# Performance work log

Hardware: AMD Instinct MI355X
Metric: run time of the kernel (lower is better)

## Reference

```python
import jax, jax.numpy as jnp
import numpy as np

B, C, H, W = 2, 192, 64, 64
HEADS, KS = 6, 7
HD = C // HEADS


def setup_inputs() -> dict:
    key = jax.random.key(0)
    ks = jax.random.split(key, 6)
    s = 0.02
    return {
        "x": jax.random.normal(ks[0], (B, C, H, W), jnp.float32),
        "W_qkv1": jax.random.normal(ks[1], (3 * C, C, 1, 1), jnp.float32) * s,
        "b_qkv1": jnp.zeros((3 * C,), jnp.float32),
        "W_qkv2": jax.random.normal(ks[2], (3 * C, 1, 3, 3), jnp.float32) * s,  # depthwise
        "b_qkv2": jnp.zeros((3 * C,), jnp.float32),
        "temperature": jnp.ones((HEADS, 1, 1, 1), jnp.float32),
        "rpb": jax.random.normal(ks[3], (HEADS, 2 * KS - 1, 2 * KS - 1), jnp.float32) * s,
        "W_proj": jax.random.normal(ks[4], (C, C, 1, 1), jnp.float32) * s,
        "b_proj": jnp.zeros((C,), jnp.float32),
    }


def _conv(x, w, b, pad, groups=1):
    y = jax.lax.conv_general_dilated(
        x, w, (1, 1), pad,
        dimension_numbers=("NCHW", "OIHW", "NCHW"),
        feature_group_count=groups)
    return y + b[None, :, None, None]


def _l2norm(t, eps=1e-12):
    n = jnp.sqrt(jnp.sum(t * t, axis=-1, keepdims=True))
    return t / jnp.maximum(n, eps)


def _nbr_idx(L, K):
    # NATTEN shifted-window neighborhood (dilation=1): window start clamped to image.
    start = jnp.clip(jnp.arange(L) - K // 2, 0, L - K)
    idx = start[:, None] + jnp.arange(K)[None, :]        # [L,K] absolute neighbor index
    rel = idx - jnp.arange(L)[:, None] + (K - 1)         # [L,K] rpb table index
    return idx, rel


def _forward(x, W_qkv1, b_qkv1, W_qkv2, b_qkv2, temperature, rpb, W_proj, b_proj):
    Bq, Cq, Hh, Ww = x.shape
    heads = rpb.shape[0]
    K = (rpb.shape[1] + 1) // 2
    hd = Cq // heads
    qkv = _conv(_conv(x, W_qkv1, b_qkv1, "VALID"), W_qkv2, b_qkv2, "SAME", groups=3 * Cq)
    qkv = qkv.reshape(Bq, 3, heads, hd, Hh, Ww).transpose(1, 0, 2, 4, 5, 3)  # [3,B,h,H,W,d]
    q, k, v = qkv[0], qkv[1], qkv[2]
    q = _l2norm(q)
    k = _l2norm(k)
    idx_i, rel_i = _nbr_idx(Hh, K)
    idx_j, rel_j = _nbr_idx(Ww, K)
    ii = idx_i[:, None, :, None]  # [H,1,K,1]
    jj = idx_j[None, :, None, :]  # [1,W,1,K] -> broadcast [H,W,K,K]
    k_nb = k[:, :, ii, jj, :]     # [B,h,H,W,K,K,d]
    attn = jnp.einsum("bhijd,bhijkld->bhijkl", q, k_nb)
    bias = rpb[:, rel_i[:, None, :, None], rel_j[None, :, None, :]]  # [h,H,W,K,K]
    attn = (attn + bias[None]) * temperature.reshape(1, heads, 1, 1, 1, 1)
    attn = jax.nn.softmax(attn.reshape(Bq, heads, Hh, Ww, K * K), axis=-1)
    v_nb = v[:, :, ii, jj, :].reshape(Bq, heads, Hh, Ww, K * K, hd)
    out = jnp.einsum("bhijk,bhijkd->bhijd", attn, v_nb)
    out = out.transpose(0, 1, 4, 2, 3).reshape(Bq, Cq, Hh, Ww)
    return _conv(out, W_proj, b_proj, "VALID")


def reference(x, W_qkv1, b_qkv1, W_qkv2, b_qkv2, temperature, rpb, W_proj, b_proj):
    return _forward(x, W_qkv1, b_qkv1, W_qkv2, b_qkv2, temperature, rpb, W_proj, b_proj)
```

## Files before the change

### kernel.cpp

```cpp
#include <hip/hip_runtime.h>
#include <math.h>

#define HW 4096

typedef __attribute__((ext_vector_type(8))) short short8;
typedef __attribute__((ext_vector_type(8))) _Float16 half8;
typedef __attribute__((ext_vector_type(4))) float floatx4;

__device__ inline float bflo(unsigned u) { return __uint_as_float(u << 16); }
__device__ inline float bfhi(unsigned u) { return __uint_as_float(u & 0xffff0000u); }
__device__ inline unsigned short f2bf(float x) {
    unsigned u = __float_as_uint(x);
    return (unsigned short)((u + 0x7fffu + ((u >> 16) & 1u)) >> 16);
}
__device__ inline unsigned f2bf2(float lo, float hi) {
    unsigned a = __float_as_uint(lo), b = __float_as_uint(hi);
    a = (a + 0x7fffu + ((a >> 16) & 1u)) >> 16;
    b = (b + 0x7fffu + ((b >> 16) & 1u)) & 0xffff0000u;
    return a | b;
}
__device__ inline unsigned short f2h(float x) {
    _Float16 h = (_Float16)x;
    return __builtin_bit_cast(unsigned short, h);
}


__global__ __launch_bounds__(256) void k_gq(const float* __restrict__ x,
    const float* __restrict__ W1, const float* __restrict__ b1,
    unsigned short* __restrict__ qkv)
{
    __shared__ __align__(16) unsigned short As[64 * 200];
    __shared__ __align__(16) unsigned short Bs[64 * 200];
    const int t = threadIdx.x;
    const int m0 = blockIdx.x * 64;
    const int n0 = blockIdx.y * 64;
    const int w = t >> 6, lane = t & 63;
    const int b = m0 >> 12, px0 = m0 & 4095;
    {
        const float* xb = x + ((size_t)(b * 192) << 12) + px0 + lane;
        const int cb = w * 48;
        #pragma unroll
        for (int r4 = 0; r4 < 12; ++r4) {
            float v0 = xb[(size_t)(cb + r4 * 4 + 0) << 12];
            float v1 = xb[(size_t)(cb + r4 * 4 + 1) << 12];
            float v2 = xb[(size_t)(cb + r4 * 4 + 2) << 12];
            float v3 = xb[(size_t)(cb + r4 * 4 + 3) << 12];
            *(uint2*)&As[lane * 200 + cb + r4 * 4] =
                make_uint2(f2bf2(v0, v1), f2bf2(v2, v3));
        }
    }
    #pragma unroll
    for (int pass = 0; pass < 12; ++pass) {
        int idx = pass * 256 + t;
        int row = idx / 48, ch = idx - row * 48;
        float4 wv = *(const float4*)&W1[(size_t)(n0 + row) * 192 + ch * 4];
        *(uint2*)&Bs[row * 200 + ch * 4] =
            make_uint2(f2bf2(wv.x, wv.y), f2bf2(wv.z, wv.w));
    }
    __syncthreads();
    const int lm = lane & 15, lq = lane >> 4;
    floatx4 acc[4] = {};
    #pragma unroll
    for (int ks = 0; ks < 6; ++ks) {
        short8 bf = *(const short8*)&Bs[(w * 16 + lm) * 200 + ks * 32 + lq * 8];
        #pragma unroll
        for (int mt = 0; mt < 4; ++mt) {
            short8 af = *(const short8*)&As[(mt * 16 + lm) * 200 + ks * 32 + lq * 8];
            acc[mt] = __builtin_amdgcn_mfma_f32_16x16x32_bf16(af, bf, acc[mt], 0, 0, 0);
        }
    }
    __syncthreads();
    const float bias = b1[n0 + w * 16 + lm];
    #pragma unroll
    for (int mt = 0; mt < 4; ++mt)
        #pragma unroll
        for (int r = 0; r < 4; ++r)
            As[(mt * 16 + lq * 4 + r) * 72 + w * 16 + lm] = f2bf(acc[mt][r] + bias);
    __syncthreads();
    #pragma unroll
    for (int pass = 0; pass < 2; ++pass) {
        int idx = pass * 256 + t;
        int m = idx >> 3, n8 = idx & 7;
        uint4 val = *(const uint4*)&As[m * 72 + n8 * 8];
        int oc = n0 + n8 * 8;
        int g = oc >> 5, d = oc & 31;
        *(uint4*)&qkv[((((size_t)(b * 18 + g) << 12) + px0 + m) << 5) + d] = val;
    }
}

__global__ __launch_bounds__(256) void k_attn(const unsigned short* __restrict__ qkv,
    const float* __restrict__ W2, const float* __restrict__ b2,
    const float* __restrict__ temp, const float* __restrict__ rpb,
    unsigned short* __restrict__ attnO)
{
    __shared__ __align__(16) char lds[49088];
    unsigned short* Ks  = (unsigned short*)lds;
    unsigned short* Ps  = (unsigned short*)lds;
    unsigned short* Vts = (unsigned short*)(lds + 29696);
    float* rpbs = (float*)(lds + 44544);
    float* dwW  = (float*)(lds + 45248);
    float* dwB  = (float*)(lds + 48704);

    const int t = threadIdx.x;
    const int head = blockIdx.y, b = blockIdx.z;

    for (int idx = t; idx < 864; idx += 256) {
        int plane = idx / 288, rem = idx - plane * 288;
        dwW[idx] = W2[(plane * 192 + head * 32 + (rem & 31)) * 9 + (rem >> 5)];
    }
    if (t < 96) dwB[t] = b2[(t >> 5) * 192 + head * 32 + (t & 31)];
    if (t < 169) rpbs[t] = rpb[head * 169 + t];
    __syncthreads();

    const int ti = blockIdx.x >> 3, tj = blockIdx.x & 7;
    const int i0 = ti * 8, j0 = tj * 8;
    const int r0 = min(max(i0 - 3, 0), 50), c0 = min(max(j0 - 3, 0), 50);
    const unsigned short* qpl = qkv + ((size_t)(b * 18 + head) << 17);
    const unsigned short* kpl = qkv + ((size_t)(b * 18 + 6 + head) << 17);
    const unsigned short* vpl = qkv + ((size_t)(b * 18 + 12 + head) << 17);

    if (t < 196) {
        int r = (t * 2341) >> 15, cc = t - r * 14;
        const int pi = r0 + r, pj = c0 + cc;
        float acc[32];
        #pragma unroll
        for (int e = 0; e < 32; ++e) acc[e] = dwB[32 + e];
        #pragma unroll
        for (int di = -1; di <= 1; ++di) {
            int ii = pi + di;
            if (ii < 0 || ii > 63) continue;
            #pragma unroll
            for (int dj = -1; dj <= 1; ++dj) {
                int jj = pj + dj;
                if (jj < 0 || jj > 63) continue;
                const float* wt = &dwW[(9 + (di + 1) * 3 + dj + 1) * 32];
                const uint4* kg = (const uint4*)(kpl + (((ii << 6) + jj) << 5));
                #pragma unroll
                for (int q = 0; q < 4; ++q) {
                    uint4 u = kg[q];
                    unsigned uu[4] = {u.x, u.y, u.z, u.w};
                    #pragma unroll
                    for (int e = 0; e < 4; ++e) {
                        acc[q * 8 + e * 2]     = fmaf(bflo(uu[e]), wt[q * 8 + e * 2],     acc[q * 8 + e * 2]);
                        acc[q * 8 + e * 2 + 1] = fmaf(bfhi(uu[e]), wt[q * 8 + e * 2 + 1], acc[q * 8 + e * 2 + 1]);
                    }
                }
            }
        }
        float ss = 0.f;
        #pragma unroll
        for (int e = 0; e < 32; ++e) ss = fmaf(acc[e], acc[e], ss);
        float rinv = 1.0f / fmaxf(sqrtf(ss), 1e-12f);
        #pragma unroll
        for (int q = 0; q < 4; ++q) {
            uint4 p;
            p.x = f2bf2(acc[q * 8 + 0] * rinv, acc[q * 8 + 1] * rinv);
            p.y = f2bf2(acc[q * 8 + 2] * rinv, acc[q * 8 + 3] * rinv);
            p.z = f2bf2(acc[q * 8 + 4] * rinv, acc[q * 8 + 5] * rinv);
            p.w = f2bf2(acc[q * 8 + 6] * rinv, acc[q * 8 + 7] * rinv);
            *(uint4*)&Ks[t * 40 + q * 8] = p;
        }
        #pragma unroll
        for (int e = 0; e < 32; ++e) acc[e] = dwB[64 + e];
        #pragma unroll
        for (int di = -1; di <= 1; ++di) {
            int ii = pi + di;
            if (ii < 0 || ii > 63) continue;
            #pragma unroll
            for (int dj = -1; dj <= 1; ++dj) {
                int jj = pj + dj;
                if (jj < 0 || jj > 63) continue;
                const float* wt = &dwW[(18 + (di + 1) * 3 + dj + 1) * 32];
                const uint4* vg = (const uint4*)(vpl + (((ii << 6) + jj) << 5));
                #pragma unroll
                for (int q = 0; q < 4; ++q) {
                    uint4 u = vg[q];
                    unsigned uu[4] = {u.x, u.y, u.z, u.w};
                    #pragma unroll
                    for (int e = 0; e < 4; ++e) {
                        acc[q * 8 + e * 2]     = fmaf(bflo(uu[e]), wt[q * 8 + e * 2],     acc[q * 8 + e * 2]);
                        acc[q * 8 + e * 2 + 1] = fmaf(bfhi(uu[e]), wt[q * 8 + e * 2 + 1], acc[q * 8 + e * 2 + 1]);
                    }
                }
            }
        }
        #pragma unroll
        for (int e = 0; e < 32; ++e) Vts[e * 232 + t] = f2h(acc[e]);
    }
    for (int idx = t; idx < 448; idx += 256) {
        int row = (idx * 2341) >> 15;
        int c = idx - row * 14;
        ((unsigned*)(Vts + row * 232))[98 + c] = 0u;
    }

    const int w = t >> 6, lane = t & 63;
    const int lm = lane & 15, lq = lane >> 4;
    const int px = w * 16 + lm;
    const int i = i0 + (px >> 3), j = j0 + (px & 7);
    float qf[8];
    #pragma unroll
    for (int e = 0; e < 8; ++e) qf[e] = dwB[lq * 8 + e];
    #pragma unroll
    for (int di = -1; di <= 1; ++di) {
        int ii = i + di;
        if (ii < 0 || ii > 63) continue;
        #pragma unroll
        for (int dj = -1; dj <= 1; ++dj) {
            int jj = j + dj;
            if (jj < 0 || jj > 63) continue;
            const float* wt = &dwW[((di + 1) * 3 + dj + 1) * 32 + lq * 8];
            uint4 u = *(const uint4*)(qpl + ((((ii << 6) + jj) << 5) + lq * 8));
            unsigned uu[4] = {u.x, u.y, u.z, u.w};
            #pragma unroll
            for (int e = 0; e < 4; ++e) {
                qf[e * 2]     = fmaf(bflo(uu[e]), wt[e * 2],     qf[e * 2]);
                qf[e * 2 + 1] = fmaf(bfhi(uu[e]), wt[e * 2 + 1], qf[e * 2 + 1]);
            }
        }
    }
    float qs = 0.f;
    #pragma unroll
    for (int e = 0; e < 8; ++e) qs = fmaf(qf[e], qf[e], qs);
    qs += __shfl_xor(qs, 16);
    qs += __shfl_xor(qs, 32);
    float qinv = 1.0f / fmaxf(sqrtf(qs), 1e-12f);
    short8 bq;
    #pragma unroll
    for (int e = 0; e < 8; ++e) bq[e] = (short)f2bf(qf[e] * qinv);
    __syncthreads();

    floatx4 acc[13];
    #pragma unroll
    for (int mt = 0; mt < 13; ++mt) {
        short8 ak = *(const short8*)&Ks[(mt * 16 + lm) * 40 + lq * 8];
        floatx4 z = {0.f, 0.f, 0.f, 0.f};
        acc[mt] = __builtin_amdgcn_mfma_f32_16x16x32_bf16(ak, bq, z, 0, 0, 0);
    }
    __syncthreads();

    const int si = min(max(i - 3, 0), 57), sj = min(max(j - 3, 0), 57);
    const int vloi = si - r0, vloj = sj - c0;
    const int oi = r0 - i + 6, oj = c0 - j + 6;
    const float th = temp[head];
    float mx = -1e30f;
    #pragma unroll
    for (int mt = 0; mt < 13; ++mt) {
        int nb0 = mt * 16 + lq * 4;
        int rh0 = (nb0 * 2341) >> 15;
        int ch0 = nb0 - rh0 * 14;
        #pragma unroll
        for (int r = 0; r < 4; ++r) {
            int ch = ch0 + r, rh = rh0;
            if (ch >= 14) { ch -= 14; rh += 1; }
            int bidx = (rh + oi) * 13 + (ch + oj);
            float bias = rpbs[max(0, min(168, bidx))];
            bool valid = ((unsigned)(rh - vloi) <= 6u) && ((unsigned)(ch - vloj) <= 6u);
            float s = (acc[mt][r] + bias) * th;
            s = valid ? s : -1e30f;
            acc[mt][r] = s;
            mx = fmaxf(mx, s);
        }
    }
    mx = fmaxf(mx, __shfl_xor(mx, 16));
    mx = fmaxf(mx, __shfl_xor(mx, 32));
    float ssum = 0.f;
    #pragma unroll
    for (int mt = 0; mt < 13; ++mt)
        #pragma unroll
        for (int r = 0; r < 4; ++r) {
            float e = __expf(acc[mt][r] - mx);
            acc[mt][r] = e;
            ssum += e;
        }
    ssum += __shfl_xor(ssum, 16);
    ssum += __shfl_xor(ssum, 32);
    const float rs = 1.0f / ssum;

    if (lane < 32) {
        uint4 z4 = {0u, 0u, 0u, 0u};
        *(uint4*)&Ps[(w * 16 + (lane >> 1)) * 232 + 208 + (lane & 1) * 8] = z4;
    }
    #pragma unroll
    for (int mt = 0; mt < 13; ++mt) {
        unsigned lo = (unsigned)f2h(acc[mt][0] * rs) | ((unsigned)f2h(acc[mt][1] * rs) << 16);
        unsigned hi = (unsigned)f2h(acc[mt][2] * rs) | ((unsigned)f2h(acc[mt][3] * rs) << 16);
        *(uint2*)&Ps[px * 232 + mt * 16 + lq * 4] = make_uint2(lo, hi);
    }
    __syncthreads();

    floatx4 oacc[2] = {};
    #pragma unroll
    for (int ks = 0; ks < 7; ++ks) {
        half8 ap = *(const half8*)&Ps[(w * 16 + lm) * 232 + ks * 32 + lq * 8];
        #pragma unroll
        for (int n2 = 0; n2 < 2; ++n2) {
            half8 bv = *(const half8*)&Vts[(n2 * 16 + lm) * 232 + ks * 32 + lq * 8];
            oacc[n2] = __builtin_amdgcn_mfma_f32_16x16x32_f16(ap, bv, oacc[n2], 0, 0, 0);
        }
    }
    #pragma unroll
    for (int n2 = 0; n2 < 2; ++n2)
        #pragma unroll
        for (int r = 0; r < 4; ++r) {
            int p2 = w * 16 + lq * 4 + r;
            int i2 = i0 + (p2 >> 3), j2 = j0 + (p2 & 7);
            attnO[((size_t)((b << 12) + (i2 << 6) + j2)) * 192 + head * 32 + n2 * 16 + lm]
                = f2bf(oacc[n2][r]);
        }
}

__global__ __launch_bounds__(256) void k_gp(const unsigned short* __restrict__ Ain,
    const float* __restrict__ Wp, const float* __restrict__ bp,
    float* __restrict__ out)
{
    __shared__ __align__(16) unsigned short As[64 * 200];
    __shared__ __align__(16) unsigned short Bs[64 * 200];
    const int t = threadIdx.x;
    const int m0 = blockIdx.x * 64;
    const int n0 = blockIdx.y * 64;
    #pragma unroll
    for (int pass = 0; pass < 6; ++pass) {
        int idx = pass * 256 + t;
        int m = idx / 24, c16 = idx % 24;
        *(uint4*)&As[m * 200 + c16 * 8] = *(const uint4*)&Ain[(size_t)(m0 + m) * 192 + c16 * 8];
    }
    #pragma unroll
    for (int pass = 0; pass < 12; ++pass) {
        int idx = pass * 256 + t;
        int row = idx / 48, ch = idx - row * 48;
        float4 wv = *(const float4*)&Wp[(size_t)(n0 + row) * 192 + ch * 4];
        *(uint2*)&Bs[row * 200 + ch * 4] =
            make_uint2(f2bf2(wv.x, wv.y), f2bf2(wv.z, wv.w));
    }
    __syncthreads();
    const int w = t >> 6, lane = t & 63;
    const int lm = lane & 15, lq = lane >> 4;
    floatx4 acc[4] = {};
    #pragma unroll
    for (int ks = 0; ks < 6; ++ks) {
        short8 bf = *(const short8*)&Bs[(w * 16 + lm) * 200 + ks * 32 + lq * 8];
        #pragma unroll
        for (int mt = 0; mt < 4; ++mt) {
            short8 af = *(const short8*)&As[(mt * 16 + lm) * 200 + ks * 32 + lq * 8];
            acc[mt] = __builtin_amdgcn_mfma_f32_16x16x32_bf16(af, bf, acc[mt], 0, 0, 0);
        }
    }
    __syncthreads();
    float* fs = (float*)As;
    const float bias = bp[n0 + w * 16 + lm];
    #pragma unroll
    for (int mt = 0; mt < 4; ++mt)
        #pragma unroll
        for (int r = 0; r < 4; ++r)
            fs[(w * 16 + lm) * 68 + mt * 16 + lq * 4 + r] = acc[mt][r] + bias;
    __syncthreads();
    const int b = m0 >> 12, px0 = m0 & 4095;
    #pragma unroll
    for (int pass = 0; pass < 4; ++pass) {
        int idx = pass * 256 + t;
        int n = idx >> 4, m4 = idx & 15;
        float4 val = *(const float4*)&fs[n * 68 + m4 * 4];
        *(float4*)&out[((size_t)(b * 192 + n0 + n) << 12) + px0 + m4 * 4] = val;
    }
}

extern "C" void kernel_launch(void* const* d_in, const int* in_sizes, int n_in,
                              void* d_out, int out_size, void* d_ws, size_t ws_size,
                              hipStream_t stream) {
    const float* x    = (const float*)d_in[0];
    const float* W1   = (const float*)d_in[1];
    const float* b1   = (const float*)d_in[2];
    const float* W2   = (const float*)d_in[3];
    const float* b2   = (const float*)d_in[4];
    const float* temp = (const float*)d_in[5];
    const float* rpb  = (const float*)d_in[6];
    const float* Wp   = (const float*)d_in[7];
    const float* bp   = (const float*)d_in[8];
    float* out = (float*)d_out;

    char* ws = (char*)d_ws;
    unsigned short* qkv1b = (unsigned short*)(ws);
    unsigned short* attnO = (unsigned short*)(ws + 9437184);

    k_gq  <<<dim3(128, 9), 256, 0, stream>>>(x, W1, b1, qkv1b);
    k_attn<<<dim3(64, 6, 2), 256, 0, stream>>>(qkv1b, W2, b2, temp, rpb, attnO);
    k_gp  <<<dim3(128, 3), 256, 0, stream>>>(attnO, Wp, bp, out);
}
```

Measured before the change: 114.8 us.

## Stage depthwise-conv halo tiles in LDS and split channels across threads

The K, V and Q depthwise 3x3 convolutions inside the attention kernel now first copy a zero-padded halo tile of the bf16 qkv planes into shared memory, in two row halves for K and V. The taps are then read from LDS instead of issuing nine overlapping global loads per pixel. Work is also split into pixel x channel-octet tasks, so 392 tasks use all 256 threads instead of 196 threads each holding 32 accumulators. The L2 norm is reduced with lane shuffles. In exchange the kernel gains several extra __syncthreads barriers and reuses part of the LDS buffer.

```diff
diff --git a/kernel.cpp b/kernel.cpp
--- a/kernel.cpp
+++ b/kernel.cpp
@@ -22,6 +22,22 @@
 __device__ inline unsigned short f2h(float x) {
     _Float16 h = (_Float16)x;
     return __builtin_bit_cast(unsigned short, h);
+}
+
+__device__ inline void stage_halo(unsigned short* raw, const unsigned short* pl,
+                                  int t, int npx, int gi0, int gj0)
+{
+    if (t < npx) {
+        int ri = t >> 4, rj = t & 15;
+        int gi = gi0 + ri, gj = gj0 + rj;
+        uint4 v0 = {0u,0u,0u,0u}, v1 = v0, v2 = v0, v3 = v0;
+        if ((unsigned)gi < 64u && (unsigned)gj < 64u) {
+            const uint4* src = (const uint4*)(pl + (((gi << 6) + gj) << 5));
+            v0 = src[0]; v1 = src[1]; v2 = src[2]; v3 = src[3];
+        }
+        uint4* d = (uint4*)&raw[t * 32];
+        d[0] = v0; d[1] = v1; d[2] = v2; d[3] = v3;
+    }
 }
 
 
@@ -96,6 +112,7 @@
     __shared__ __align__(16) char lds[49088];
     unsigned short* Ks  = (unsigned short*)lds;
     unsigned short* Ps  = (unsigned short*)lds;
+    unsigned short* raw = (unsigned short*)(lds + 16640);
     unsigned short* Vts = (unsigned short*)(lds + 29696);
     float* rpbs = (float*)(lds + 44544);
     float* dwW  = (float*)(lds + 45248);
@@ -103,15 +120,6 @@
 
     const int t = threadIdx.x;
     const int head = blockIdx.y, b = blockIdx.z;
-
-    for (int idx = t; idx < 864; idx += 256) {
-        int plane = idx / 288, rem = idx - plane * 288;
-        dwW[idx] = W2[(plane * 192 + head * 32 + (rem & 31)) * 9 + (rem >> 5)];
-    }
-    if (t < 96) dwB[t] = b2[(t >> 5) * 192 + head * 32 + (t & 31)];
-    if (t < 169) rpbs[t] = rpb[head * 169 + t];
-    __syncthreads();
-
     const int ti = blockIdx.x >> 3, tj = blockIdx.x & 7;
     const int i0 = ti * 8, j0 = tj * 8;
     const int r0 = min(max(i0 - 3, 0), 50), c0 = min(max(j0 - 3, 0), 50);
@@ -119,103 +127,108 @@
     const unsigned short* kpl = qkv + ((size_t)(b * 18 + 6 + head) << 17);
     const unsigned short* vpl = qkv + ((size_t)(b * 18 + 12 + head) << 17);
 
-    if (t < 196) {
-        int r = (t * 2341) >> 15, cc = t - r * 14;
-        const int pi = r0 + r, pj = c0 + cc;
-        float acc[32];
-        #pragma unroll
-        for (int e = 0; e < 32; ++e) acc[e] = dwB[32 + e];
-        #pragma unroll
-        for (int di = -1; di <= 1; ++di) {
-            int ii = pi + di;
-            if (ii < 0 || ii > 63) continue;
-            #pragma unroll
-            for (int dj = -1; dj <= 1; ++dj) {
-                int jj = pj + dj;
-                if (jj < 0 || jj > 63) continue;
-                const float* wt = &dwW[(9 + (di + 1) * 3 + dj + 1) * 32];
-                const uint4* kg = (const uint4*)(kpl + (((ii << 6) + jj) << 5));
-                #pragma unroll
-                for (int q = 0; q < 4; ++q) {
-                    uint4 u = kg[q];
-                    unsigned uu[4] = {u.x, u.y, u.z, u.w};
-                    #pragma unroll
-                    for (int e = 0; e < 4; ++e) {
-                        acc[q * 8 + e * 2]     = fmaf(bflo(uu[e]), wt[q * 8 + e * 2],     acc[q * 8 + e * 2]);
-                        acc[q * 8 + e * 2 + 1] = fmaf(bfhi(uu[e]), wt[q * 8 + e * 2 + 1], acc[q * 8 + e * 2 + 1]);
-                    }
-                }
-            }
-        }
-        float ss = 0.f;
-        #pragma unroll
-        for (int e = 0; e < 32; ++e) ss = fmaf(acc[e], acc[e], ss);
-        float rinv = 1.0f / fmaxf(sqrtf(ss), 1e-12f);
-        #pragma unroll
-        for (int q = 0; q < 4; ++q) {
-            uint4 p;
-            p.x = f2bf2(acc[q * 8 + 0] * rinv, acc[q * 8 + 1] * rinv);
-            p.y = f2bf2(acc[q * 8 + 2] * rinv, acc[q * 8 + 3] * rinv);
-            p.z = f2bf2(acc[q * 8 + 4] * rinv, acc[q * 8 + 5] * rinv);
-            p.w = f2bf2(acc[q * 8 + 6] * rinv, acc[q * 8 + 7] * rinv);
-            *(uint4*)&Ks[t * 40 + q * 8] = p;
-        }
-        #pragma unroll
-        for (int e = 0; e < 32; ++e) acc[e] = dwB[64 + e];
-        #pragma unroll
-        for (int di = -1; di <= 1; ++di) {
-            int ii = pi + di;
-            if (ii < 0 || ii > 63) continue;
-            #pragma unroll
-            for (int dj = -1; dj <= 1; ++dj) {
-                int jj = pj + dj;
-                if (jj < 0 || jj > 63) continue;
-                const float* wt = &dwW[(18 + (di + 1) * 3 + dj + 1) * 32];
-                const uint4* vg = (const uint4*)(vpl + (((ii << 6) + jj) << 5));
-                #pragma unroll
-                for (int q = 0; q < 4; ++q) {
-                    uint4 u = vg[q];
-                    unsigned uu[4] = {u.x, u.y, u.z, u.w};
-                    #pragma unroll
-                    for (int e = 0; e < 4; ++e) {
-                        acc[q * 8 + e * 2]     = fmaf(bflo(uu[e]), wt[q * 8 + e * 2],     acc[q * 8 + e * 2]);
-                        acc[q * 8 + e * 2 + 1] = fmaf(bfhi(uu[e]), wt[q * 8 + e * 2 + 1], acc[q * 8 + e * 2 + 1]);
-                    }
-                }
-            }
-        }
-        #pragma unroll
-        for (int e = 0; e < 32; ++e) Vts[e * 232 + t] = f2h(acc[e]);
-    }
+    for (int idx = t; idx < 864; idx += 256) {
+        int plane = idx / 288, rem = idx - plane * 288;
+        dwW[idx] = W2[(plane * 192 + head * 32 + (rem & 31)) * 9 + (rem >> 5)];
+    }
+    if (t < 96) dwB[t] = b2[(t >> 5) * 192 + head * 32 + (t & 31)];
+    if (t < 169) rpbs[t] = rpb[head * 169 + t];
     for (int idx = t; idx < 448; idx += 256) {
         int row = (idx * 2341) >> 15;
         int c = idx - row * 14;
         ((unsigned*)(Vts + row * 232))[98 + c] = 0u;
     }
 
+    for (int h = 0; h < 2; ++h) {
+        stage_halo(raw, kpl, t, 144, r0 - 1 + h * 7, c0 - 1);
+        __syncthreads();
+        for (int s = 0; s < 2; ++s) {
+            int task = s * 256 + t;
+            if (task < 392) {
+                int px = task >> 2, oct = task & 3;
+                int rl = (px * 2341) >> 15, cc = px - rl * 14;
+                float a[8];
+                #pragma unroll
+                for (int e = 0; e < 8; ++e) a[e] = dwB[32 + oct * 8 + e];
+                #pragma unroll
+                for (int tap = 0; tap < 9; ++tap) {
+                    uint4 u = *(const uint4*)&raw[((rl + tap / 3) * 16 + cc + tap % 3) * 32 + oct * 8];
+                    const float* wt = &dwW[(9 + tap) * 32 + oct * 8];
+                    unsigned uu[4] = {u.x, u.y, u.z, u.w};
+                    #pragma unroll
+                    for (int e = 0; e < 4; ++e) {
+                        a[e * 2]     = fmaf(bflo(uu[e]), wt[e * 2],     a[e * 2]);
+                        a[e * 2 + 1] = fmaf(bfhi(uu[e]), wt[e * 2 + 1], a[e * 2 + 1]);
+                    }
+                }
+                float ss = 0.f;
+                #pragma unroll
+                for (int e = 0; e < 8; ++e) ss = fmaf(a[e], a[e], ss);
+                ss += __shfl_xor(ss, 1);
+                ss += __shfl_xor(ss, 2);
+                float rinv = 1.0f / fmaxf(sqrtf(ss), 1e-12f);
+                int pxk = (h * 7 + rl) * 14 + cc;
+                uint4 p;
+                p.x = f2bf2(a[0] * rinv, a[1] * rinv);
+                p.y = f2bf2(a[2] * rinv, a[3] * rinv);
+                p.z = f2bf2(a[4] * rinv, a[5] * rinv);
+                p.w = f2bf2(a[6] * rinv, a[7] * rinv);
+                *(uint4*)&Ks[pxk * 40 + oct * 8] = p;
+            }
+        }
+        __syncthreads();
+    }
+
+    for (int h = 0; h < 2; ++h) {
+        stage_halo(raw, vpl, t, 144, r0 - 1 + h * 7, c0 - 1);
+        __syncthreads();
+        for (int s = 0; s < 2; ++s) {
+            int task = s * 256 + t;
+            if (task < 392) {
+                int px = task >> 2, oct = task & 3;
+                int rl = (px * 2341) >> 15, cc = px - rl * 14;
+                float a[8];
+                #pragma unroll
+                for (int e = 0; e < 8; ++e) a[e] = dwB[64 + oct * 8 + e];
+                #pragma unroll
+                for (int tap = 0; tap < 9; ++tap) {
+                    uint4 u = *(const uint4*)&raw[((rl + tap / 3) * 16 + cc + tap % 3) * 32 + oct * 8];
+                    const float* wt = &dwW[(18 + tap) * 32 + oct * 8];
+                    unsigned uu[4] = {u.x, u.y, u.z, u.w};
+                    #pragma unroll
+                    for (int e = 0; e < 4; ++e) {
+                        a[e * 2]     = fmaf(bflo(uu[e]), wt[e * 2],     a[e * 2]);
+                        a[e * 2 + 1] = fmaf(bfhi(uu[e]), wt[e * 2 + 1], a[e * 2 + 1]);
+                    }
+                }
+                int pxk = (h * 7 + rl) * 14 + cc;
+                #pragma unroll
+                for (int e = 0; e < 8; ++e)
+                    Vts[(oct * 8 + e) * 232 + pxk] = f2h(a[e]);
+            }
+        }
+        __syncthreads();
+    }
+
+    stage_halo(raw, qpl, t, 160, i0 - 1, c0 - 1);
+    __syncthreads();
     const int w = t >> 6, lane = t & 63;
     const int lm = lane & 15, lq = lane >> 4;
     const int px = w * 16 + lm;
     const int i = i0 + (px >> 3), j = j0 + (px & 7);
+    const int qrow = px >> 3, qcol = (px & 7) + (j0 - c0);
     float qf[8];
     #pragma unroll
     for (int e = 0; e < 8; ++e) qf[e] = dwB[lq * 8 + e];
     #pragma unroll
-    for (int di = -1; di <= 1; ++di) {
-        int ii = i + di;
-        if (ii < 0 || ii > 63) continue;
-        #pragma unroll
-        for (int dj = -1; dj <= 1; ++dj) {
-            int jj = j + dj;
-            if (jj < 0 || jj > 63) continue;
-            const float* wt = &dwW[((di + 1) * 3 + dj + 1) * 32 + lq * 8];
-            uint4 u = *(const uint4*)(qpl + ((((ii << 6) + jj) << 5) + lq * 8));
-            unsigned uu[4] = {u.x, u.y, u.z, u.w};
-            #pragma unroll
-            for (int e = 0; e < 4; ++e) {
-                qf[e * 2]     = fmaf(bflo(uu[e]), wt[e * 2],     qf[e * 2]);
-                qf[e * 2 + 1] = fmaf(bfhi(uu[e]), wt[e * 2 + 1], qf[e * 2 + 1]);
-            }
+    for (int tap = 0; tap < 9; ++tap) {
+        uint4 u = *(const uint4*)&raw[((qrow + tap / 3) * 16 + qcol + tap % 3) * 32 + lq * 8];
+        const float* wt = &dwW[tap * 32 + lq * 8];
+        unsigned uu[4] = {u.x, u.y, u.z, u.w};
+        #pragma unroll
+        for (int e = 0; e < 4; ++e) {
+            qf[e * 2]     = fmaf(bflo(uu[e]), wt[e * 2],     qf[e * 2]);
+            qf[e * 2 + 1] = fmaf(bfhi(uu[e]), wt[e * 2 + 1], qf[e * 2 + 1]);
         }
     }
     float qs = 0.f;
```

Measured after the change: 115.7 us. No clear change (+0.8%).
